# Performance work log

Hardware: AMD Instinct MI355X
Metric: run time of the kernel (lower is better)

## Reference

```python
import jax, jax.numpy as jnp
import numpy as np
from functools import partial

EPS = 1e-12  # F.normalize eps (clamp_min on the norm)


def conv2d(x, w, b, groups=1):
    # x: [B, Cin, H, W], w: [Cout, Cin//groups, 3, 3], 'same' padding, stride 1
    y = jax.lax.conv_general_dilated(
        x, w, window_strides=(1, 1), padding='SAME',
        dimension_numbers=('NCHW', 'OIHW', 'NCHW'),
        feature_group_count=groups)
    return y + b[None, :, None, None]


def setup_inputs() -> dict:
    key = jax.random.key(0)
    ks = jax.random.split(key, 8)
    B, C, H, W = 16, 256, 32, 32
    HW = H * W
    T = 2  # tasks: seg, depth
    return {
        'features_seg': jax.random.normal(ks[0], (B, C, H, W), jnp.float32),
        'features_depth': jax.random.normal(ks[1], (B, C, H, W), jnp.float32),
        'proj_w_seg': jax.random.normal(ks[2], (C, C, 3, 3), jnp.float32) * 0.02,
        'proj_b_seg': jnp.zeros((C,), jnp.float32),
        'proj_w_depth': jax.random.normal(ks[3], (C, C, 3, 3), jnp.float32) * 0.02,
        'proj_b_depth': jnp.zeros((C,), jnp.float32),
        'fusion_w': jax.random.normal(ks[4], (HW, T, 3, 3), jnp.float32) * 0.02,
        'fusion_b': jnp.zeros((HW,), jnp.float32),
    }


def reference(features_seg, features_depth, proj_w_seg, proj_b_seg,
              proj_w_depth, proj_b_depth, fusion_w, fusion_b):
    gamma = 0.5
    feats = [features_seg, features_depth]
    proj = [(proj_w_seg, proj_b_seg), (proj_w_depth, proj_b_depth)]
    B, C, H, W = features_seg.shape
    HW = H * W

    # Per-task cosine-similarity affinity matrices [B, HW, HW]
    Ms = []
    for f in feats:
        fv = f.reshape(B, C, HW)
        fn = fv / jnp.maximum(jnp.linalg.norm(fv, axis=1, keepdims=True), EPS)
        aff = jnp.einsum('bci,bcj->bij', fn, fn)  # [B, HW, HW]
        Ms.append(aff.reshape(B, HW, H, W))

    # Stack on dim=2 then flatten -> interleaved channels [B, HW*T, H, W]
    M = jnp.stack(Ms, axis=2).reshape(B, -1, H, W)
    M = conv2d(M, fusion_w, fusion_b, groups=HW)  # [B, HW, H, W]

    attention = M.reshape(B, HW, HW).transpose(0, 2, 1)  # [B, HW, HW]

    outs = []
    for f, (w, b) in zip(feats, proj):
        value = conv2d(f, w, b).reshape(B, C, HW)          # [B, C, HW]
        attended = jnp.einsum('bck,bkj->bcj', value, attention)
        attended = attended.reshape(B, C, H, W)
        outs.append(gamma * attended + (1.0 - gamma) * f)
    return tuple(outs)
```

## Files before the change

kernel.cpp:

```cpp
#include <hip/hip_runtime.h>
#include <hip/hip_bf16.h>

typedef __bf16 bf16;
typedef __attribute__((ext_vector_type(8))) __bf16 bf16x8;
typedef __attribute__((ext_vector_type(4))) __bf16 bf16x4v;
typedef __attribute__((ext_vector_type(4))) float f32x4;

#define B_  16
#define C_  256
#define HW_ 1024
#define PADR 1156
#define ZSTR 295936

__device__ __forceinline__ void gll16(const bf16* g, bf16* l) {
  __builtin_amdgcn_global_load_lds((const __attribute__((address_space(1))) void*)g,
                                   (__attribute__((address_space(3))) void*)l, 16, 0, 0);
}

__global__ void prep_kernel(const float* __restrict__ f0, const float* __restrict__ f1,
                            bf16* __restrict__ fTpad, float* __restrict__ rn) {
  __shared__ float sm[256][33];
  __shared__ float ps[8][32];
  int z = blockIdx.y, t = z >> 4, b = z & 15;
  int k0 = blockIdx.x * 32;
  int tid = threadIdx.x;
  const float* fb = (t ? f1 : f0) + (size_t)b * C_ * HW_ + k0;
  int kk = tid & 31, cg = tid >> 5;
  float ssq = 0.f;
  #pragma unroll
  for (int i = 0; i < 32; ++i) {
    int c = cg + i * 8;
    float v = fb[(size_t)c * HW_ + kk];
    sm[c][kk] = v;
    ssq += v * v;
  }
  ps[cg][kk] = ssq;

  bf16x8 zv;
  #pragma unroll
  for (int e = 0; e < 8; ++e) zv[e] = (bf16)0.f;
  if (tid < 64) {
    int c = (tid & 31) * 8, side = tid >> 5;
    *(bf16x8*)(fTpad + ((size_t)z * PADR + (blockIdx.x + 1) * 34 + side * 33) * C_ + c) = zv;
  }
  if (blockIdx.x == 0 || blockIdx.x == 31) {
    int prow = (blockIdx.x == 0) ? 0 : 33;
    for (int q = tid; q < 34 * 32; q += 256) {
      int wcol = q >> 5, c = (q & 31) * 8;
      *(bf16x8*)(fTpad + ((size_t)z * PADR + prow * 34 + wcol) * C_ + c) = zv;
    }
  }

  __syncthreads();
  if (tid < 32) {
    float s = 0.f;
    #pragma unroll
    for (int r = 0; r < 8; ++r) s += ps[r][tid];
    rn[z * 1024 + k0 + tid] = 1.f / fmaxf(sqrtf(s), 1e-12f);
  }
  int wl = tid >> 3, c0 = (tid & 7) * 32;
  bf16* dst = fTpad + ((size_t)z * PADR + (blockIdx.x + 1) * 34 + wl + 1) * C_ + c0;
  #pragma unroll
  for (int u = 0; u < 4; ++u) {
    bf16x8 vv;
    #pragma unroll
    for (int e = 0; e < 8; ++e) vv[e] = (bf16)sm[c0 + u * 8 + e][wl];
    *(bf16x8*)(dst + u * 8) = vv;
  }
}

__global__ void fusion_conv2(const bf16* __restrict__ aff, const float* __restrict__ fw,
                             const float* __restrict__ fb, bf16* __restrict__ M) {
  __shared__ float sa[2][1024];
  int bi = blockIdx.x;
  int i = bi & 1023, b = bi >> 10;
  int tid = threadIdx.x;
  #pragma unroll
  for (int t = 0; t < 2; ++t) {
    const bf16* arow = aff + (((size_t)t * 16 + b) * 1024 + i) * 1024;
    bf16x4v ch = ((const bf16x4v*)arow)[tid];
    sa[t][tid * 4 + 0] = (float)ch[0];
    sa[t][tid * 4 + 1] = (float)ch[1];
    sa[t][tid * 4 + 2] = (float)ch[2];
    sa[t][tid * 4 + 3] = (float)ch[3];
  }
  float wgt[2][9];
  #pragma unroll
  for (int t = 0; t < 2; ++t)
    #pragma unroll
    for (int q = 0; q < 9; ++q) wgt[t][q] = fw[i * 18 + t * 9 + q];
  float bias = fb[i];
  __syncthreads();
  #pragma unroll
  for (int s0 = 0; s0 < 4; ++s0) {
    int s = tid + s0 * 256;
    int h = s >> 5, w = s & 31;
    float acc = bias;
    #pragma unroll
    for (int kh = 0; kh < 3; ++kh) {
      int hh = h + kh - 1;
      if ((unsigned)hh < 32u) {
        #pragma unroll
        for (int kw = 0; kw < 3; ++kw) {
          int ww = w + kw - 1;
          if ((unsigned)ww < 32u) {
            acc += wgt[0][kh * 3 + kw] * sa[0][hh * 32 + ww];
            acc += wgt[1][kh * 3 + kw] * sa[1][hh * 32 + ww];
          }
        }
      }
    }
    M[((size_t)bi << 10) + s] = (bf16)acc;
  }
}

__global__ void reorder_w(const float* __restrict__ w0, const float* __restrict__ w1,
                          bf16* __restrict__ y) {
  int i = blockIdx.x * 256 + threadIdx.x;
  int t = i / 589824, r2 = i % 589824;
  int c = r2 / 2304, r = r2 % 2304;
  int cin = r / 9, d = r % 9;
  y[(size_t)t * 589824 + c * 2304 + d * 256 + cin] = (bf16)(t ? w1 : w0)[r2];
}

template<int MODE>
__global__ __launch_bounds__(256, 4)
void gemm_nt(const bf16* __restrict__ A, long long sA,
             const bf16* __restrict__ Bm, long long sB, int K,
             bf16* __restrict__ Cb, long long sC,
             const float* __restrict__ x0, const float* __restrict__ x1,
             float* __restrict__ Co) {
  __shared__ bf16 As[128 * 64];
  __shared__ bf16 Bs[128 * 64];
  const int z = blockIdx.z;
  const int tt = (MODE == 1) ? (z >> 4) : (z & 1);
  const int bb = (MODE == 1) ? (z & 15) : (z >> 1);
  const int zold = tt * 16 + bb;
  const bf16* Ab = A + (size_t)(MODE == 3 ? tt : z) * sA;
  const bf16* Bb = Bm + (size_t)(MODE == 1 ? z : (MODE == 2 ? bb : zold)) * sB;
  const int m0 = blockIdx.y * 128, n0 = blockIdx.x * 128;
  const int tid = threadIdx.x;
  const int lane = tid & 63, wave = tid >> 6;
  const int wm = (wave >> 1) * 64, wn = (wave & 1) * 64;
  const int fr = lane & 15, fq = lane >> 4;

  const bf16* srcA[4];
  const bf16* srcB[4];
  int ldsA[4], ldsB[4];
  #pragma unroll
  for (int s = 0; s < 4; ++s) {
    int q = (wave * 4 + s) * 64 + lane;
    int row = q >> 3, c = (q & 7) ^ (row & 7);
    ldsA[s] = ldsB[s] = __builtin_amdgcn_readfirstlane((wave * 4 + s) * 512);
    if (MODE == 1) {
      int j = m0 + row;
      srcA[s] = Ab + (size_t)(((j >> 5) + 1) * 34 + (j & 31) + 1) * C_ + c * 8;
    } else {
      srcA[s] = Ab + (size_t)(m0 + row) * K + c * 8;
    }
    int jb = n0 + row;
    if (MODE == 1) {
      srcB[s] = Bb + (size_t)(((jb >> 5) + 1) * 34 + (jb & 31) + 1) * C_ + c * 8;
    } else if (MODE == 3) {
      srcB[s] = Bb + (size_t)(((jb >> 5) + 1) * 34 + (jb & 31) + 1) * C_ + c * 8;
    } else {
      srcB[s] = Bb + (size_t)jb * K + c * 8;
    }
  }
  int lA[2][4], lB[2][4];
  #pragma unroll
  for (int h = 0; h < 2; ++h) {
    #pragma unroll
    for (int i = 0; i < 4; ++i) {
      int rr = wm + i * 16 + fr;
      lA[h][i] = rr * 64 + (((h * 4) + fq) ^ (rr & 7)) * 8;
      int rc = wn + i * 16 + fr;
      lB[h][i] = rc * 64 + (((h * 4) + fq) ^ (rc & 7)) * 8;
    }
  }

  f32x4 acc[4][4];
  #pragma unroll
  for (int i = 0; i < 4; ++i)
    #pragma unroll
    for (int j = 0; j < 4; ++j) acc[i][j] = 0.f;

  for (int k0 = 0; k0 < K; k0 += 64) {
    int boff;
    if (MODE == 3) {
      int d = k0 >> 8;
      int kh = d / 3, kw = d % 3;
      boff = ((kh - 1) * 34 + (kw - 1)) * C_ + (k0 & 255);
    } else {
      boff = k0;
    }
    #pragma unroll
    for (int s = 0; s < 4; ++s) gll16(srcA[s] + k0, As + ldsA[s]);
    #pragma unroll
    for (int s = 0; s < 4; ++s) gll16(srcB[s] + boff, Bs + ldsB[s]);
    __syncthreads();
    #pragma unroll
    for (int h = 0; h < 2; ++h) {
      bf16x8 af[4], bfr[4];
      #pragma unroll
      for (int i = 0; i < 4; ++i) af[i] = *(const bf16x8*)(&As[lA[h][i]]);
      #pragma unroll
      for (int j = 0; j < 4; ++j) bfr[j] = *(const bf16x8*)(&Bs[lB[h][j]]);
      #pragma unroll
      for (int i = 0; i < 4; ++i)
        #pragma unroll
        for (int j = 0; j < 4; ++j)
          acc[i][j] = __builtin_amdgcn_mfma_f32_16x16x32_bf16(af[i], bfr[j], acc[i][j], 0, 0, 0);
    }
    __syncthreads();
  }

  #pragma unroll
  for (int i = 0; i < 4; ++i) {
    int rbase = m0 + wm + i * 16 + fq * 4;
    #pragma unroll
    for (int j = 0; j < 4; ++j) {
      int col = n0 + wn + j * 16 + fr;
      float cj = (MODE == 1) ? x0[(size_t)z * 1024 + col] : 0.f;
      #pragma unroll
      for (int r = 0; r < 4; ++r) {
        int row = rbase + r;
        float v = acc[i][j][r];
        if (MODE == 1) {
          Cb[(size_t)z * sC + (size_t)row * 1024 + col] =
              (bf16)(v * x0[(size_t)z * 1024 + row] * cj);
        } else if (MODE == 3) {
          const float* bias = tt ? x1 : x0;
          Cb[(size_t)z * sC + (size_t)row * 1024 + col] = (bf16)(v + bias[row]);
        } else {
          const float* fp = tt ? x1 : x0;
          Co[(size_t)zold * sC + (size_t)row * 1024 + col] =
              0.5f * v + 0.5f * fp[(size_t)bb * sC + (size_t)row * 1024 + col];
        }
      }
    }
  }
}

extern "C" void kernel_launch(void* const* d_in, const int* in_sizes, int n_in,
                              void* d_out, int out_size, void* d_ws, size_t ws_size,
                              hipStream_t stream) {
  const float* f0 = (const float*)d_in[0];
  const float* f1 = (const float*)d_in[1];
  const float* w0 = (const float*)d_in[2];
  const float* b0 = (const float*)d_in[3];
  const float* w1 = (const float*)d_in[4];
  const float* b1 = (const float*)d_in[5];
  const float* fusion_w = (const float*)d_in[6];
  const float* fusion_b = (const float*)d_in[7];
  float* out = (float*)d_out;

  char* ws = (char*)d_ws;
  bf16* aff   = (bf16*)ws;
  bf16* Mbuf  = (bf16*)ws;
  bf16* Wr    = (bf16*)(ws + 33554432ull);
  bf16* value = (bf16*)(ws + 35913728ull);
  bf16* fTpad = (bf16*)(ws + 67108864ull);
  float* rn   = (float*)(ws + 86048768ull);

  prep_kernel<<<dim3(32, 32), 256, 0, stream>>>(f0, f1, fTpad, rn);
  gemm_nt<1><<<dim3(8, 8, 32), 256, 0, stream>>>(
      fTpad, ZSTR, fTpad, ZSTR, C_,
      aff, (long long)HW_ * HW_, rn, rn, nullptr);
  fusion_conv2<<<16384, 256, 0, stream>>>(aff, fusion_w, fusion_b, Mbuf);
  reorder_w<<<4608, 256, 0, stream>>>(w0, w1, Wr);
  gemm_nt<3><<<dim3(8, 2, 32), 256, 0, stream>>>(
      Wr, 589824LL, fTpad, ZSTR, 2304,
      value, (long long)C_ * HW_, b0, b1, nullptr);
  gemm_nt<2><<<dim3(8, 2, 32), 256, 0, stream>>>(
      value, (long long)C_ * HW_, Mbuf, (long long)HW_ * HW_, 1024,
      nullptr, (long long)C_ * HW_, f0, f1, out);
}
```

Baseline: 239.8 us.

## Merge prep with weight reorder and affinity GEMM with value conv GEMM

Folds the weight-reorder work into the feature-prep launch as extra blocks, and merges the affinity GEMM and the value-projection conv GEMM into one launch that dispatches on block index. This cuts the launch count from six to four and lets independent work fill the GPU together, reducing tail idle time between small kernels. The workspace layout moves so that value and Wr no longer overlap aff, which now stays live in the same launch. In exchange, the combined kernels share one register and LDS budget, and their block mixes are less uniform.

Result: slower. 247.0 us (+3.0%).

```diff
diff --git a/kernel.cpp b/kernel.cpp
--- a/kernel.cpp
+++ b/kernel.cpp
@@ -17,13 +17,24 @@
                                    (__attribute__((address_space(3))) void*)l, 16, 0, 0);
 }
 
-__global__ void prep_kernel(const float* __restrict__ f0, const float* __restrict__ f1,
-                            bf16* __restrict__ fTpad, float* __restrict__ rn) {
+__global__ void prep_fat(const float* __restrict__ f0, const float* __restrict__ f1,
+                         const float* __restrict__ w0, const float* __restrict__ w1,
+                         bf16* __restrict__ fTpad, float* __restrict__ rn,
+                         bf16* __restrict__ Wr) {
+  int tid = threadIdx.x;
+  if (blockIdx.x >= 1024) {
+    int i = (blockIdx.x - 1024) * 256 + tid;
+    int t = i / 589824, r2 = i % 589824;
+    int c = r2 / 2304, r = r2 % 2304;
+    int cin = r / 9, d = r % 9;
+    Wr[(size_t)t * 589824 + c * 2304 + d * 256 + cin] = (bf16)(t ? w1 : w0)[r2];
+    return;
+  }
   __shared__ float sm[256][33];
   __shared__ float ps[8][32];
-  int z = blockIdx.y, t = z >> 4, b = z & 15;
-  int k0 = blockIdx.x * 32;
-  int tid = threadIdx.x;
+  int bx = blockIdx.x & 31, z = blockIdx.x >> 5;
+  int t = z >> 4, b = z & 15;
+  int k0 = bx * 32;
   const float* fb = (t ? f1 : f0) + (size_t)b * C_ * HW_ + k0;
   int kk = tid & 31, cg = tid >> 5;
   float ssq = 0.f;
@@ -41,10 +52,10 @@
   for (int e = 0; e < 8; ++e) zv[e] = (bf16)0.f;
   if (tid < 64) {
     int c = (tid & 31) * 8, side = tid >> 5;
-    *(bf16x8*)(fTpad + ((size_t)z * PADR + (blockIdx.x + 1) * 34 + side * 33) * C_ + c) = zv;
-  }
-  if (blockIdx.x == 0 || blockIdx.x == 31) {
-    int prow = (blockIdx.x == 0) ? 0 : 33;
+    *(bf16x8*)(fTpad + ((size_t)z * PADR + (bx + 1) * 34 + side * 33) * C_ + c) = zv;
+  }
+  if (bx == 0 || bx == 31) {
+    int prow = (bx == 0) ? 0 : 33;
     for (int q = tid; q < 34 * 32; q += 256) {
       int wcol = q >> 5, c = (q & 31) * 8;
       *(bf16x8*)(fTpad + ((size_t)z * PADR + prow * 34 + wcol) * C_ + c) = zv;
@@ -59,7 +70,7 @@
     rn[z * 1024 + k0 + tid] = 1.f / fmaxf(sqrtf(s), 1e-12f);
   }
   int wl = tid >> 3, c0 = (tid & 7) * 32;
-  bf16* dst = fTpad + ((size_t)z * PADR + (blockIdx.x + 1) * 34 + wl + 1) * C_ + c0;
+  bf16* dst = fTpad + ((size_t)z * PADR + (bx + 1) * 34 + wl + 1) * C_ + c0;
   #pragma unroll
   for (int u = 0; u < 4; ++u) {
     bf16x8 vv;
@@ -114,31 +125,20 @@
   }
 }
 
-__global__ void reorder_w(const float* __restrict__ w0, const float* __restrict__ w1,
-                          bf16* __restrict__ y) {
-  int i = blockIdx.x * 256 + threadIdx.x;
-  int t = i / 589824, r2 = i % 589824;
-  int c = r2 / 2304, r = r2 % 2304;
-  int cin = r / 9, d = r % 9;
-  y[(size_t)t * 589824 + c * 2304 + d * 256 + cin] = (bf16)(t ? w1 : w0)[r2];
-}
-
 template<int MODE>
-__global__ __launch_bounds__(256, 4)
-void gemm_nt(const bf16* __restrict__ A, long long sA,
-             const bf16* __restrict__ Bm, long long sB, int K,
-             bf16* __restrict__ Cb, long long sC,
-             const float* __restrict__ x0, const float* __restrict__ x1,
-             float* __restrict__ Co) {
-  __shared__ bf16 As[128 * 64];
-  __shared__ bf16 Bs[128 * 64];
-  const int z = blockIdx.z;
+__device__ __forceinline__
+void gemm_core(int bx, int by, int z, bf16* As, bf16* Bs,
+               const bf16* __restrict__ A, long long sA,
+               const bf16* __restrict__ Bm, long long sB, int K,
+               bf16* __restrict__ Cb, long long sC,
+               const float* __restrict__ x0, const float* __restrict__ x1,
+               float* __restrict__ Co) {
   const int tt = (MODE == 1) ? (z >> 4) : (z & 1);
   const int bb = (MODE == 1) ? (z & 15) : (z >> 1);
   const int zold = tt * 16 + bb;
   const bf16* Ab = A + (size_t)(MODE == 3 ? tt : z) * sA;
   const bf16* Bb = Bm + (size_t)(MODE == 1 ? z : (MODE == 2 ? bb : zold)) * sB;
-  const int m0 = blockIdx.y * 128, n0 = blockIdx.x * 128;
+  const int m0 = by * 128, n0 = bx * 128;
   const int tid = threadIdx.x;
   const int lane = tid & 63, wave = tid >> 6;
   const int wm = (wave >> 1) * 64, wn = (wave & 1) * 64;
@@ -159,9 +159,7 @@
       srcA[s] = Ab + (size_t)(m0 + row) * K + c * 8;
     }
     int jb = n0 + row;
-    if (MODE == 1) {
-      srcB[s] = Bb + (size_t)(((jb >> 5) + 1) * 34 + (jb & 31) + 1) * C_ + c * 8;
-    } else if (MODE == 3) {
+    if (MODE == 1 || MODE == 3) {
       srcB[s] = Bb + (size_t)(((jb >> 5) + 1) * 34 + (jb & 31) + 1) * C_ + c * 8;
     } else {
       srcB[s] = Bb + (size_t)jb * K + c * 8;
@@ -242,6 +240,37 @@
   }
 }
 
+__global__ __launch_bounds__(256, 4)
+void gemm_fat(const bf16* __restrict__ fTpad, const float* __restrict__ rn,
+              bf16* __restrict__ aff, const bf16* __restrict__ Wr,
+              bf16* __restrict__ value, const float* __restrict__ b0,
+              const float* __restrict__ b1) {
+  __shared__ bf16 As[128 * 64];
+  __shared__ bf16 Bs[128 * 64];
+  int blk = blockIdx.x;
+  if (blk < 2048) {
+    gemm_core<1>(blk & 7, (blk >> 3) & 7, blk >> 6, As, Bs,
+                 fTpad, ZSTR, fTpad, ZSTR, C_,
+                 aff, (long long)HW_ * HW_, rn, rn, nullptr);
+  } else {
+    int q = blk - 2048;
+    gemm_core<3>(q & 7, (q >> 3) & 1, q >> 4, As, Bs,
+                 Wr, 589824LL, fTpad, ZSTR, 2304,
+                 value, (long long)C_ * HW_, b0, b1, nullptr);
+  }
+}
+
+__global__ __launch_bounds__(256, 4)
+void gemm_attend(const bf16* __restrict__ value, const bf16* __restrict__ Mbuf,
+                 const float* __restrict__ f0, const float* __restrict__ f1,
+                 float* __restrict__ out) {
+  __shared__ bf16 As[128 * 64];
+  __shared__ bf16 Bs[128 * 64];
+  gemm_core<2>(blockIdx.x, blockIdx.y, blockIdx.z, As, Bs,
+               value, (long long)C_ * HW_, Mbuf, (long long)HW_ * HW_, 1024,
+               nullptr, (long long)C_ * HW_, f0, f1, out);
+}
+
 extern "C" void kernel_launch(void* const* d_in, const int* in_sizes, int n_in,
                               void* d_out, int out_size, void* d_ws, size_t ws_size,
                               hipStream_t stream) {
@@ -258,21 +287,13 @@
   char* ws = (char*)d_ws;
   bf16* aff   = (bf16*)ws;
   bf16* Mbuf  = (bf16*)ws;
-  bf16* Wr    = (bf16*)(ws + 33554432ull);
-  bf16* value = (bf16*)(ws + 35913728ull);
   bf16* fTpad = (bf16*)(ws + 67108864ull);
-  float* rn   = (float*)(ws + 86048768ull);
-
-  prep_kernel<<<dim3(32, 32), 256, 0, stream>>>(f0, f1, fTpad, rn);
-  gemm_nt<1><<<dim3(8, 8, 32), 256, 0, stream>>>(
-      fTpad, ZSTR, fTpad, ZSTR, C_,
-      aff, (long long)HW_ * HW_, rn, rn, nullptr);
+  bf16* Wr    = (bf16*)(ws + 86048768ull);
+  bf16* value = (bf16*)(ws + 88408064ull);
+  float* rn   = (float*)(ws + 105185280ull);
+
+  prep_fat<<<5632, 256, 0, stream>>>(f0, f1, w0, w1, fTpad, rn, Wr);
+  gemm_fat<<<2560, 256, 0, stream>>>(fTpad, rn, aff, Wr, value, b0, b1);
   fusion_conv2<<<16384, 256, 0, stream>>>(aff, fusion_w, fusion_b, Mbuf);
-  reorder_w<<<4608, 256, 0, stream>>>(w0, w1, Wr);
-  gemm_nt<3><<<dim3(8, 2, 32), 256, 0, stream>>>(
-      Wr, 589824LL, fTpad, ZSTR, 2304,
-      value, (long long)C_ * HW_, b0, b1, nullptr);
-  gemm_nt<2><<<dim3(8, 2, 32), 256, 0, stream>>>(
-      value, (long long)C_ * HW_, Mbuf, (long long)HW_ * HW_, 1024,
-      nullptr, (long long)C_ * HW_, f0, f1, out);
-}
+  gemm_attend<<<dim3(8, 2, 32), 256, 0, stream>>>(value, Mbuf, f0, f1, out);
+}
```
